# Kernel tuning notes

Hardware: AMD Instinct MI355X
Metric: run time of the kernel (lower is better)

The kernel has to match this reference:

```python
import jax, jax.numpy as jnp
import numpy as np

N = 50000          # num_nodes
E = 800000         # general (base) edge count
R_BASE = 3         # base relation types
R = 2 * R_BASE + 1 # base + inverse + self-loop relation
D_IN = 64
D_HID = 64
D_OUT = 64


def _glorot(k, shape):
    # xavier_uniform with relu gain, fan over last two dims
    gain = np.sqrt(2.0)
    bound = gain * np.sqrt(6.0 / (shape[-2] + shape[-1]))
    return jax.random.uniform(k, shape, jnp.float32, -bound, bound)


def setup_inputs() -> dict:
    key = jax.random.key(0)
    ks = jax.random.split(key, 6)
    x = jax.random.normal(ks[0], (N, D_IN), dtype=jnp.float32)
    src = jax.random.randint(ks[1], (E,), 0, N)
    dst = jax.random.randint(ks[2], (E,), 0, N)
    et = jax.random.randint(ks[3], (E,), 0, R_BASE)
    nodes = jnp.arange(N)
    # triples = [original edges, inverse edges (type+R_BASE), self-loops (type 2*R_BASE)]
    triples = jnp.concatenate([
        jnp.stack([src, et, dst], axis=1),
        jnp.stack([dst, et + R_BASE, src], axis=1),
        jnp.stack([nodes, jnp.full((N,), 2 * R_BASE), nodes], axis=1),
    ], axis=0).astype(jnp.int64)
    w1 = _glorot(ks[4], (R, D_IN, D_HID))
    w2 = _glorot(ks[5], (R, D_HID, D_OUT))
    b1 = jnp.zeros((D_HID,), jnp.float32)
    b2 = jnp.zeros((D_OUT,), jnp.float32)
    return {"x": x, "w1": w1, "b1": b1, "w2": w2, "b2": b2,
            "triples": triples, "num_nodes": N, "num_edge_types": R}


def _rgcn_layer(x, W, b, triples, num_nodes, num_rels):
    # vertical stacking: sparse adj [R*N, N], entry (r*N+src, dst) = 1, row-normalised
    src, et, dst = triples[:, 0], triples[:, 1], triples[:, 2]
    rows = et * num_nodes + src                     # [T] row index in stacked adj
    counts = jnp.zeros((num_rels * num_nodes,), x.dtype).at[rows].add(1.0)
    vals = 1.0 / counts[rows]                       # per-edge row-normalised weight
    msgs = vals[:, None] * x[dst]                   # [T, d] gathered + scaled messages
    af = jax.ops.segment_sum(msgs, rows, num_segments=num_rels * num_nodes)
    af = af.reshape(num_rels, num_nodes, x.shape[1])  # [R, N, d]
    return jnp.einsum('rio,rni->no', W, af) + b


def reference(x, w1, b1, w2, b2, triples, num_nodes, num_edge_types):
    h = _rgcn_layer(x, w1, b1, triples, num_nodes, num_edge_types)
    h = jax.nn.relu(h)
    out = _rgcn_layer(h, w2, b2, triples, num_nodes, num_edge_types)
    return out
```

## Files before the change

kernel.cpp:

```cpp
#include <hip/hip_runtime.h>
#include <stdint.h>

#define D 64
#define TILE 2048
#define PK 8
#define NBMAX 128
#define BW 512
#define RMAX 8

typedef __attribute__((ext_vector_type(8))) short bf16x8;
typedef __attribute__((ext_vector_type(4))) float f32x4;

__device__ __forceinline__ unsigned short f2bf(float f) {
    union { float f; unsigned int i; } v; v.f = f;
    unsigned int x = v.i;
    unsigned int r = (x + 0x7FFFu + ((x >> 16) & 1u)) >> 16;
    return (unsigned short)r;
}
__device__ __forceinline__ float lo_bf(unsigned int u) {
    union { unsigned int i; float f; } v; v.i = u << 16; return v.f;
}
__device__ __forceinline__ float hi_bf(unsigned int u) {
    union { unsigned int i; float f; } v; v.i = u & 0xFFFF0000u; return v.f;
}

__global__ void detect_kernel(const int* __restrict__ t32, int probe, int expect,
                              unsigned int* __restrict__ flag) {
    if (blockIdx.x == 0 && threadIdx.x == 0)
        flag[0] = (t32[probe] == expect) ? 0u : 1u;
}

__global__ void __launch_bounds__(256) binpass_kernel(const unsigned int* __restrict__ t32,
                                                      const unsigned int* __restrict__ flag,
                                                      unsigned int* __restrict__ staging,
                                                      unsigned int* __restrict__ binCnt,
                                                      int M, int NB, int CAP) {
    __shared__ unsigned int sorted[TILE];
    __shared__ unsigned char sortedb[TILE];
    __shared__ unsigned int hist[NBMAX];
    __shared__ unsigned int scan_[NBMAX];
    __shared__ unsigned int cur[NBMAX];
    __shared__ unsigned int gbase[NBMAX];

    int tid = threadIdx.x;
    int tileBase = blockIdx.x * TILE;

    for (int i = tid; i < NBMAX; i += 256) hist[i] = 0;
    __syncthreads();

    bool is64 = flag[0] != 0;
    unsigned int myE[PK];
    unsigned char myB[PK];
    #pragma unroll
    for (int k = 0; k < PK; k++) {
        int e = tileBase + tid * PK + k;
        myB[k] = 0xFF;
        if (e < M) {
            long w = (long)e * 3;
            unsigned int src, et, dst;
            if (is64) { src = t32[2*w]; et = t32[2*(w+1)]; dst = t32[2*(w+2)]; }
            else      { src = t32[w];   et = t32[w+1];     dst = t32[w+2]; }
            unsigned int b = src >> 9;
            unsigned int lsrc = src & (BW - 1);
            myE[k] = (lsrc << 20) | (et << 17) | dst;
            myB[k] = (unsigned char)b;
            atomicAdd(&hist[b], 1u);
        }
    }
    __syncthreads();

    if (tid < NBMAX) scan_[tid] = hist[tid];
    __syncthreads();
    for (int off = 1; off < NBMAX; off <<= 1) {
        unsigned int v = (tid < NBMAX && tid >= off) ? scan_[tid - off] : 0u;
        __syncthreads();
        if (tid < NBMAX) scan_[tid] += v;
        __syncthreads();
    }
    if (tid < NB) {
        gbase[tid] = atomicAdd(&binCnt[tid], hist[tid]);
        cur[tid] = scan_[tid] - hist[tid];
    }
    __syncthreads();

    #pragma unroll
    for (int k = 0; k < PK; k++) {
        if (myB[k] != 0xFF) {
            unsigned int p = atomicAdd(&cur[myB[k]], 1u);
            sorted[p] = myE[k];
            sortedb[p] = myB[k];
        }
    }
    __syncthreads();

    unsigned int total = scan_[NB - 1];
    for (unsigned int i = tid; i < total; i += 256) {
        unsigned int b = sortedb[i];
        unsigned int local = i - (scan_[b] - hist[b]);
        unsigned int slot = gbase[b] + local;
        if (slot < (unsigned int)CAP)
            staging[(size_t)b * CAP + slot] = sorted[i];
    }
}

__global__ void __launch_bounds__(512) buildcsr_kernel(const unsigned int* __restrict__ staging,
                                                       const unsigned int* __restrict__ binCnt,
                                                       unsigned int* __restrict__ segOff,
                                                       uint2* __restrict__ adj,
                                                       int M, int N, int R, int NB, int CAP) {
    __shared__ unsigned int hist7[RMAX * BW];
    __shared__ unsigned int curs7[RMAX * BW];
    __shared__ unsigned int scanbuf[BW];
    __shared__ unsigned int sbase[NBMAX];

    int b = blockIdx.x, tid = threadIdx.x;
    int nodeBase = b * BW;
    int nNodes = N - nodeBase; if (nNodes > BW) nNodes = BW;
    unsigned int cntB = binCnt[b]; if (cntB > (unsigned int)CAP) cntB = CAP;

    for (int i = tid; i < RMAX * BW; i += 512) hist7[i] = 0;
    __syncthreads();

    const unsigned int* st = staging + (size_t)b * CAP;
    for (unsigned int i = tid; i < cntB; i += 512) {
        unsigned int e = st[i];
        unsigned int lsrc = e >> 20, et = (e >> 17) & 7u;
        atomicAdd(&hist7[et * BW + lsrc], 1u);
    }
    __syncthreads();

    unsigned int d = 0;
    for (int r2 = 0; r2 < R; r2++) d += hist7[r2 * BW + tid];
    scanbuf[tid] = d;
    __syncthreads();
    for (int off = 1; off < BW; off <<= 1) {
        unsigned int v = (tid >= off) ? scanbuf[tid - off] : 0u;
        __syncthreads();
        scanbuf[tid] += v;
        __syncthreads();
    }

    if (tid < NBMAX) sbase[tid] = (tid < NB) ? min(binCnt[tid], (unsigned int)CAP) : 0u;
    __syncthreads();
    for (int off = 1; off < NBMAX; off <<= 1) {
        unsigned int v = (tid < NBMAX && tid >= off) ? sbase[tid - off] : 0u;
        __syncthreads();
        if (tid < NBMAX) sbase[tid] += v;
        __syncthreads();
    }
    unsigned int baseB = (b == 0) ? 0u : sbase[b - 1];

    unsigned int nodeStart = baseB + scanbuf[tid] - d;
    if (tid < nNodes) {
        unsigned int o = nodeStart;
        for (int et = 0; et < R; et++) {
            segOff[(size_t)(nodeBase + tid) * 8 + et] = o;
            curs7[et * BW + tid] = o;
            o += hist7[et * BW + tid];
        }
        segOff[(size_t)(nodeBase + tid) * 8 + R] = o;
    } else {
        for (int et = 0; et < R; et++) curs7[et * BW + tid] = 0;
    }
    __syncthreads();

    for (unsigned int i = tid; i < cntB; i += 512) {
        unsigned int e = st[i];
        unsigned int lsrc = e >> 20, et = (e >> 17) & 7u, dst = e & 0x1FFFFu;
        unsigned int pos = atomicAdd(&curs7[et * BW + lsrc], 1u);
        float val = 1.0f / (float)hist7[et * BW + lsrc];
        uint2 m; m.x = dst; m.y = __float_as_uint(val);
        adj[pos] = m;
    }
}

__global__ void convert_kernel(const float* __restrict__ x, unsigned short* __restrict__ xb, int total) {
    int i = (blockIdx.x * blockDim.x + threadIdx.x) * 4;
    if (i + 3 < total) {
        float4 v = *(const float4*)(x + i);
        ushort4 o; o.x = f2bf(v.x); o.y = f2bf(v.y); o.z = f2bf(v.z); o.w = f2bf(v.w);
        *(ushort4*)(xb + i) = o;
    } else {
        for (int j = i; j < total; j++) xb[j] = f2bf(x[j]);
    }
}

__global__ void packw_kernel(const float* __restrict__ W, unsigned short* __restrict__ wpack, int R) {
    int gid = blockIdx.x * blockDim.x + threadIdx.x;
    if (gid >= R * 512) return;
    int lane = gid & 63;
    int c = (gid >> 6) & 3;
    int t = (gid >> 8) & 1;
    int r = gid >> 9;
    int col = c * 16 + (lane & 15);
    int kbase = t * 32 + 8 * (lane >> 4);
    #pragma unroll
    for (int j = 0; j < 8; j++) {
        wpack[(size_t)gid * 8 + j] = f2bf(W[((size_t)r * D + kbase + j) * D + col]);
    }
}

template<int RM>
__global__ void __launch_bounds__(256) agg_kernel(const unsigned short* __restrict__ xtab,
                                                  const uint2* __restrict__ adj,
                                                  const unsigned int* __restrict__ segOff,
                                                  unsigned int* __restrict__ afcat,
                                                  int N, int totalWaves) {
    int w = blockIdx.x * 4 + (threadIdx.x >> 6);
    int lane = threadIdx.x & 63;
    int g = lane >> 4;
    int cq = lane & 15;
    const int stride = RM * 32;
    const int PERG = (2 * RM + 3) >> 2;
    int npairs = (N + 1) >> 1;

    for (int p = w; p < npairs; p += totalWaves) {
        int n0 = 2 * p;
        #pragma unroll
        for (int k = 0; k < PERG; k++) {
            int sidx = g * PERG + k;
            int node = n0 + (sidx >= RM ? 1 : 0);
            int r = sidx - (sidx >= RM ? RM : 0);
            bool valid = node < N;
            unsigned int s = 0, e = 0;
            if (valid) {
                s = segOff[(size_t)node * 8 + r];
                e = segOff[(size_t)node * 8 + r + 1];
            }
            float a0 = 0.f, a1 = 0.f, a2 = 0.f, a3 = 0.f;
            #pragma unroll 2
            for (unsigned int idx = s; idx < e; ++idx) {
                uint2 m = adj[idx];
                float val = __uint_as_float(m.y);
                uint2 u = *(const uint2*)(xtab + (size_t)m.x * D + 4 * cq);
                a0 += val * lo_bf(u.x);
                a1 += val * hi_bf(u.x);
                a2 += val * lo_bf(u.y);
                a3 += val * hi_bf(u.y);
            }
            if (valid) {
                uint2 o;
                o.x = ((unsigned int)f2bf(a1) << 16) | (unsigned int)f2bf(a0);
                o.y = ((unsigned int)f2bf(a3) << 16) | (unsigned int)f2bf(a2);
                *(uint2*)(afcat + (size_t)node * stride + r * 32 + 2 * cq) = o;
            }
        }
    }
}

__global__ void __launch_bounds__(256) agg_kernel_dyn(const unsigned short* __restrict__ xtab,
                                                      const uint2* __restrict__ adj,
                                                      const unsigned int* __restrict__ segOff,
                                                      unsigned int* __restrict__ afcat,
                                                      int N, int totalWaves, int Rm1) {
    int w = blockIdx.x * 4 + (threadIdx.x >> 6);
    int lane = threadIdx.x & 63;
    int g = lane >> 4;
    int cq = lane & 15;
    int stride = Rm1 * 32;
    int PERG = (2 * Rm1 + 3) >> 2;
    int npairs = (N + 1) >> 1;

    for (int p = w; p < npairs; p += totalWaves) {
        int n0 = 2 * p;
        for (int k = 0; k < PERG; k++) {
            int sidx = g * PERG + k;
            int node = n0 + (sidx >= Rm1 ? 1 : 0);
            int r = sidx - (sidx >= Rm1 ? Rm1 : 0);
            bool valid = (node < N) && (sidx < 2 * Rm1);
            unsigned int s = 0, e = 0;
            if (valid) {
                s = segOff[(size_t)node * 8 + r];
                e = segOff[(size_t)node * 8 + r + 1];
            }
            float a0 = 0.f, a1 = 0.f, a2 = 0.f, a3 = 0.f;
            for (unsigned int idx = s; idx < e; ++idx) {
                uint2 m = adj[idx];
                float val = __uint_as_float(m.y);
                uint2 u = *(const uint2*)(xtab + (size_t)m.x * D + 4 * cq);
                a0 += val * lo_bf(u.x);
                a1 += val * hi_bf(u.x);
                a2 += val * lo_bf(u.y);
                a3 += val * hi_bf(u.y);
            }
            if (valid) {
                uint2 o;
                o.x = ((unsigned int)f2bf(a1) << 16) | (unsigned int)f2bf(a0);
                o.y = ((unsigned int)f2bf(a3) << 16) | (unsigned int)f2bf(a2);
                *(uint2*)(afcat + (size_t)node * stride + r * 32 + 2 * cq) = o;
            }
        }
    }
}

__global__ void __launch_bounds__(256) gemm2_kernel(const unsigned short* __restrict__ afcat,
                                                    const unsigned short* __restrict__ xtab,
                                                    const unsigned short* __restrict__ wpack,
                                                    const float* __restrict__ bias,
                                                    unsigned short* __restrict__ out_bf,
                                                    float* __restrict__ out_f32,
                                                    int N, int nchunks, int mode) {
    int wid = blockIdx.x * 4 + (threadIdx.x >> 6);
    int lane = threadIdx.x & 63;
    if (wid >= nchunks) return;
    int n0 = wid * 16;
    int arow = n0 + (lane & 15);
    if (arow >= N) arow = N - 1;
    int ksub = 8 * (lane >> 4);

    bf16x8 a[14];
    const unsigned short* af = afcat + (size_t)arow * 384 + ksub;
    #pragma unroll
    for (int kt = 0; kt < 12; kt++) a[kt] = *(const bf16x8*)(af + kt * 32);
    const unsigned short* xr = xtab + (size_t)arow * D + ksub;
    a[12] = *(const bf16x8*)(xr);
    a[13] = *(const bf16x8*)(xr + 32);

    const unsigned short* wp = wpack + (size_t)lane * 8;
    int colb = lane & 15;
    int rowbase = n0 + (lane >> 4) * 4;
    #pragma unroll
    for (int c = 0; c < 4; c++) {
        f32x4 acc = {0.f, 0.f, 0.f, 0.f};
        #pragma unroll
        for (int kt = 0; kt < 14; kt++) {
            bf16x8 bfr = *(const bf16x8*)(wp + (size_t)(kt * 4 + c) * 512);
            acc = __builtin_amdgcn_mfma_f32_16x16x32_bf16(a[kt], bfr, acc, 0, 0, 0);
        }
        int col = 16 * c + colb;
        float bl = bias[col];
        #pragma unroll
        for (int q = 0; q < 4; q++) {
            int row = rowbase + q;
            if (row < N) {
                float o = acc[q] + bl;
                if (mode == 0) out_bf[(size_t)row * D + col] = f2bf(fmaxf(o, 0.f));
                else           out_f32[(size_t)row * D + col] = o;
            }
        }
    }
}

extern "C" void kernel_launch(void* const* d_in, const int* in_sizes, int n_in,
                              void* d_out, int out_size, void* d_ws, size_t ws_size,
                              hipStream_t stream) {
    const float* x  = (const float*)d_in[0];
    const float* w1 = (const float*)d_in[1];
    const float* b1 = (const float*)d_in[2];
    const float* w2 = (const float*)d_in[3];
    const float* b2 = (const float*)d_in[4];
    const int* trip = (const int*)d_in[5];

    const int N = in_sizes[0] / D;
    const int R = in_sizes[1] / (D * D);
    const int M = in_sizes[5] / 3;

    const int NB = (N + BW - 1) / BW;
    const int CAP = (((2 * (M / NB)) + 1023) / 1024) * 1024;

    char* p = (char*)d_ws;
    auto alloc = [&](size_t bytes) { void* q = (void*)p; p += (bytes + 255) / 256 * 256; return q; };
    unsigned int* binCnt  = (unsigned int*)alloc((size_t)NBMAX * 4);
    unsigned int* segOff  = (unsigned int*)alloc((size_t)N * 8 * 4);
    unsigned int* flag    = (unsigned int*)alloc(256);
    unsigned int* staging = (unsigned int*)alloc((size_t)NB * CAP * 4);
    uint2*        adj     = (uint2*)alloc((size_t)M * 8);
    unsigned int* afcat   = (unsigned int*)alloc((size_t)N * (R - 1) * 32 * 4);
    unsigned short* xb    = (unsigned short*)alloc((size_t)N * D * 2);
    unsigned short* hb    = (unsigned short*)alloc((size_t)N * D * 2);
    unsigned short* wp1   = (unsigned short*)alloc((size_t)R * 512 * 8 * 2);
    unsigned short* wp2   = (unsigned short*)alloc((size_t)R * 512 * 8 * 2);

    hipMemsetAsync(binCnt, 0, (size_t)NBMAX * 4, stream);

    int probe = (M - N) * 3 + 1;
    detect_kernel<<<1, 1, 0, stream>>>(trip, probe, R - 1, flag);

    int tiles = (M + TILE - 1) / TILE;
    binpass_kernel<<<tiles, 256, 0, stream>>>((const unsigned int*)trip, flag, staging, binCnt, M, NB, CAP);
    buildcsr_kernel<<<NB, 512, 0, stream>>>(staging, binCnt, segOff, adj, M, N, R, NB, CAP);

    int totX = N * D;
    convert_kernel<<<(totX / 4 + 255) / 256, 256, 0, stream>>>(x, xb, totX);
    packw_kernel<<<(R * 512 + 255) / 256, 256, 0, stream>>>(w1, wp1, R);
    packw_kernel<<<(R * 512 + 255) / 256, 256, 0, stream>>>(w2, wp2, R);

    int gblocks = 2048, tw = gblocks * 4;
    int nchunks = (N + 15) / 16;
    int gemmb = (nchunks + 3) / 4;

    if (R - 1 == 6)
        agg_kernel<6><<<gblocks, 256, 0, stream>>>(xb, adj, segOff, afcat, N, tw);
    else
        agg_kernel_dyn<<<gblocks, 256, 0, stream>>>(xb, adj, segOff, afcat, N, tw, R - 1);
    gemm2_kernel<<<gemmb, 256, 0, stream>>>((const unsigned short*)afcat, xb, wp1, b1, hb, nullptr, N, nchunks, 0);

    if (R - 1 == 6)
        agg_kernel<6><<<gblocks, 256, 0, stream>>>(hb, adj, segOff, afcat, N, tw);
    else
        agg_kernel_dyn<<<gblocks, 256, 0, stream>>>(hb, adj, segOff, afcat, N, tw, R - 1);
    gemm2_kernel<<<gemmb, 256, 0, stream>>>((const unsigned short*)afcat, hb, wp2, b2, nullptr, (float*)d_out, N, nchunks, 1);
}
```

Baseline: 286.5 us.

## Split feature tables into column halves and drop per-edge weights from adjacency

```diff
diff --git a/kernel.cpp b/kernel.cpp
--- a/kernel.cpp
+++ b/kernel.cpp
@@ -106,7 +106,7 @@
 __global__ void __launch_bounds__(512) buildcsr_kernel(const unsigned int* __restrict__ staging,
                                                        const unsigned int* __restrict__ binCnt,
                                                        unsigned int* __restrict__ segOff,
-                                                       uint2* __restrict__ adj,
+                                                       unsigned int* __restrict__ adj,
                                                        int M, int N, int R, int NB, int CAP) {
     __shared__ unsigned int hist7[RMAX * BW];
     __shared__ unsigned int curs7[RMAX * BW];
@@ -168,21 +168,20 @@
         unsigned int e = st[i];
         unsigned int lsrc = e >> 20, et = (e >> 17) & 7u, dst = e & 0x1FFFFu;
         unsigned int pos = atomicAdd(&curs7[et * BW + lsrc], 1u);
-        float val = 1.0f / (float)hist7[et * BW + lsrc];
-        uint2 m; m.x = dst; m.y = __float_as_uint(val);
-        adj[pos] = m;
-    }
-}
-
-__global__ void convert_kernel(const float* __restrict__ x, unsigned short* __restrict__ xb, int total) {
-    int i = (blockIdx.x * blockDim.x + threadIdx.x) * 4;
-    if (i + 3 < total) {
-        float4 v = *(const float4*)(x + i);
-        ushort4 o; o.x = f2bf(v.x); o.y = f2bf(v.y); o.z = f2bf(v.z); o.w = f2bf(v.w);
-        *(ushort4*)(xb + i) = o;
-    } else {
-        for (int j = i; j < total; j++) xb[j] = f2bf(x[j]);
-    }
+        adj[pos] = dst;
+    }
+}
+
+__global__ void convert_split_kernel(const float* __restrict__ x,
+                                     unsigned short* __restrict__ xbL,
+                                     unsigned short* __restrict__ xbH, int N) {
+    int gid = blockIdx.x * blockDim.x + threadIdx.x;
+    if (gid >= N * 16) return;
+    int n = gid >> 4, half = (gid >> 3) & 1, q = gid & 7;
+    float4 v = *(const float4*)(x + (size_t)n * 64 + half * 32 + q * 4);
+    ushort4 o; o.x = f2bf(v.x); o.y = f2bf(v.y); o.z = f2bf(v.z); o.w = f2bf(v.w);
+    unsigned short* dst = half ? xbH : xbL;
+    *(ushort4*)(dst + (size_t)n * 32 + q * 4) = o;
 }
 
 __global__ void packw_kernel(const float* __restrict__ W, unsigned short* __restrict__ wpack, int R) {
@@ -201,17 +200,17 @@
 }
 
 template<int RM>
-__global__ void __launch_bounds__(256) agg_kernel(const unsigned short* __restrict__ xtab,
-                                                  const uint2* __restrict__ adj,
+__global__ void __launch_bounds__(256) agg_kernel(const unsigned short* __restrict__ xh,
+                                                  const unsigned int* __restrict__ adj,
                                                   const unsigned int* __restrict__ segOff,
-                                                  unsigned int* __restrict__ afcat,
+                                                  unsigned int* __restrict__ afh,
                                                   int N, int totalWaves) {
     int w = blockIdx.x * 4 + (threadIdx.x >> 6);
     int lane = threadIdx.x & 63;
     int g = lane >> 4;
     int cq = lane & 15;
+    const int PERG = (2 * RM + 3) >> 2;
     const int stride = RM * 32;
-    const int PERG = (2 * RM + 3) >> 2;
     int npairs = (N + 1) >> 1;
 
     for (int p = w; p < npairs; p += totalWaves) {
@@ -227,38 +226,34 @@
                 s = segOff[(size_t)node * 8 + r];
                 e = segOff[(size_t)node * 8 + r + 1];
             }
-            float a0 = 0.f, a1 = 0.f, a2 = 0.f, a3 = 0.f;
-            #pragma unroll 2
+            float a0 = 0.f, a1 = 0.f;
+            #pragma unroll 4
             for (unsigned int idx = s; idx < e; ++idx) {
-                uint2 m = adj[idx];
-                float val = __uint_as_float(m.y);
-                uint2 u = *(const uint2*)(xtab + (size_t)m.x * D + 4 * cq);
-                a0 += val * lo_bf(u.x);
-                a1 += val * hi_bf(u.x);
-                a2 += val * lo_bf(u.y);
-                a3 += val * hi_bf(u.y);
+                unsigned int dst = __builtin_nontemporal_load(&adj[idx]);
+                unsigned int u = *(const unsigned int*)(xh + (size_t)dst * 32 + 2 * cq);
+                a0 += lo_bf(u);
+                a1 += hi_bf(u);
             }
             if (valid) {
-                uint2 o;
-                o.x = ((unsigned int)f2bf(a1) << 16) | (unsigned int)f2bf(a0);
-                o.y = ((unsigned int)f2bf(a3) << 16) | (unsigned int)f2bf(a2);
-                *(uint2*)(afcat + (size_t)node * stride + r * 32 + 2 * cq) = o;
-            }
-        }
-    }
-}
-
-__global__ void __launch_bounds__(256) agg_kernel_dyn(const unsigned short* __restrict__ xtab,
-                                                      const uint2* __restrict__ adj,
+                float val = (e > s) ? 1.0f / (float)(e - s) : 0.f;
+                unsigned int o = ((unsigned int)f2bf(a1 * val) << 16) | (unsigned int)f2bf(a0 * val);
+                __builtin_nontemporal_store(o, &afh[(size_t)node * stride + 32 * r + cq]);
+            }
+        }
+    }
+}
+
+__global__ void __launch_bounds__(256) agg_kernel_dyn(const unsigned short* __restrict__ xh,
+                                                      const unsigned int* __restrict__ adj,
                                                       const unsigned int* __restrict__ segOff,
-                                                      unsigned int* __restrict__ afcat,
+                                                      unsigned int* __restrict__ afh,
                                                       int N, int totalWaves, int Rm1) {
     int w = blockIdx.x * 4 + (threadIdx.x >> 6);
     int lane = threadIdx.x & 63;
     int g = lane >> 4;
     int cq = lane & 15;
+    int PERG = (2 * Rm1 + 3) >> 2;
     int stride = Rm1 * 32;
-    int PERG = (2 * Rm1 + 3) >> 2;
     int npairs = (N + 1) >> 1;
 
     for (int p = w; p < npairs; p += totalWaves) {
@@ -273,31 +268,29 @@
                 s = segOff[(size_t)node * 8 + r];
                 e = segOff[(size_t)node * 8 + r + 1];
             }
-            float a0 = 0.f, a1 = 0.f, a2 = 0.f, a3 = 0.f;
+            float a0 = 0.f, a1 = 0.f;
             for (unsigned int idx = s; idx < e; ++idx) {
-                uint2 m = adj[idx];
-                float val = __uint_as_float(m.y);
-                uint2 u = *(const uint2*)(xtab + (size_t)m.x * D + 4 * cq);
-                a0 += val * lo_bf(u.x);
-                a1 += val * hi_bf(u.x);
-                a2 += val * lo_bf(u.y);
-                a3 += val * hi_bf(u.y);
+                unsigned int dst = adj[idx];
+                unsigned int u = *(const unsigned int*)(xh + (size_t)dst * 32 + 2 * cq);
+                a0 += lo_bf(u);
+                a1 += hi_bf(u);
             }
             if (valid) {
-                uint2 o;
-                o.x = ((unsigned int)f2bf(a1) << 16) | (unsigned int)f2bf(a0);
-                o.y = ((unsigned int)f2bf(a3) << 16) | (unsigned int)f2bf(a2);
-                *(uint2*)(afcat + (size_t)node * stride + r * 32 + 2 * cq) = o;
+                float val = (e > s) ? 1.0f / (float)(e - s) : 0.f;
+                unsigned int o = ((unsigned int)f2bf(a1 * val) << 16) | (unsigned int)f2bf(a0 * val);
+                afh[(size_t)node * stride + 32 * r + cq] = o;
             }
         }
     }
 }
 
 __global__ void __launch_bounds__(256) gemm2_kernel(const unsigned short* __restrict__ afcat,
-                                                    const unsigned short* __restrict__ xtab,
+                                                    const unsigned short* __restrict__ xbL,
+                                                    const unsigned short* __restrict__ xbH,
                                                     const unsigned short* __restrict__ wpack,
                                                     const float* __restrict__ bias,
-                                                    unsigned short* __restrict__ out_bf,
+                                                    unsigned short* __restrict__ outL,
+                                                    unsigned short* __restrict__ outH,
                                                     float* __restrict__ out_f32,
                                                     int N, int nchunks, int mode) {
     int wid = blockIdx.x * 4 + (threadIdx.x >> 6);
@@ -312,9 +305,8 @@
     const unsigned short* af = afcat + (size_t)arow * 384 + ksub;
     #pragma unroll
     for (int kt = 0; kt < 12; kt++) a[kt] = *(const bf16x8*)(af + kt * 32);
-    const unsigned short* xr = xtab + (size_t)arow * D + ksub;
-    a[12] = *(const bf16x8*)(xr);
-    a[13] = *(const bf16x8*)(xr + 32);
+    a[12] = *(const bf16x8*)(xbL + (size_t)arow * 32 + ksub);
+    a[13] = *(const bf16x8*)(xbH + (size_t)arow * 32 + ksub);
 
     const unsigned short* wp = wpack + (size_t)lane * 8;
     int colb = lane & 15;
@@ -334,8 +326,12 @@
             int row = rowbase + q;
             if (row < N) {
                 float o = acc[q] + bl;
-                if (mode == 0) out_bf[(size_t)row * D + col] = f2bf(fmaxf(o, 0.f));
-                else           out_f32[(size_t)row * D + col] = o;
+                if (mode == 0) {
+                    unsigned short* dst = (c < 2) ? outL : outH;
+                    dst[(size_t)row * 32 + (col & 31)] = f2bf(fmaxf(o, 0.f));
+                } else {
+                    out_f32[(size_t)row * D + col] = o;
+                }
             }
         }
     }
@@ -364,10 +360,12 @@
     unsigned int* segOff  = (unsigned int*)alloc((size_t)N * 8 * 4);
     unsigned int* flag    = (unsigned int*)alloc(256);
     unsigned int* staging = (unsigned int*)alloc((size_t)NB * CAP * 4);
-    uint2*        adj     = (uint2*)alloc((size_t)M * 8);
+    unsigned int* adj     = (unsigned int*)alloc((size_t)M * 4);
     unsigned int* afcat   = (unsigned int*)alloc((size_t)N * (R - 1) * 32 * 4);
-    unsigned short* xb    = (unsigned short*)alloc((size_t)N * D * 2);
-    unsigned short* hb    = (unsigned short*)alloc((size_t)N * D * 2);
+    unsigned short* xbL   = (unsigned short*)alloc((size_t)N * 32 * 2);
+    unsigned short* xbH   = (unsigned short*)alloc((size_t)N * 32 * 2);
+    unsigned short* hbL   = (unsigned short*)alloc((size_t)N * 32 * 2);
+    unsigned short* hbH   = (unsigned short*)alloc((size_t)N * 32 * 2);
     unsigned short* wp1   = (unsigned short*)alloc((size_t)R * 512 * 8 * 2);
     unsigned short* wp2   = (unsigned short*)alloc((size_t)R * 512 * 8 * 2);
 
@@ -380,8 +378,7 @@
     binpass_kernel<<<tiles, 256, 0, stream>>>((const unsigned int*)trip, flag, staging, binCnt, M, NB, CAP);
     buildcsr_kernel<<<NB, 512, 0, stream>>>(staging, binCnt, segOff, adj, M, N, R, NB, CAP);
 
-    int totX = N * D;
-    convert_kernel<<<(totX / 4 + 255) / 256, 256, 0, stream>>>(x, xb, totX);
+    convert_split_kernel<<<(N * 16 + 255) / 256, 256, 0, stream>>>(x, xbL, xbH, N);
     packw_kernel<<<(R * 512 + 255) / 256, 256, 0, stream>>>(w1, wp1, R);
     packw_kernel<<<(R * 512 + 255) / 256, 256, 0, stream>>>(w2, wp2, R);
 
@@ -389,15 +386,23 @@
     int nchunks = (N + 15) / 16;
     int gemmb = (nchunks + 3) / 4;
 
-    if (R - 1 == 6)
-        agg_kernel<6><<<gblocks, 256, 0, stream>>>(xb, adj, segOff, afcat, N, tw);
-    else
-        agg_kernel_dyn<<<gblocks, 256, 0, stream>>>(xb, adj, segOff, afcat, N, tw, R - 1);
-    gemm2_kernel<<<gemmb, 256, 0, stream>>>((const unsigned short*)afcat, xb, wp1, b1, hb, nullptr, N, nchunks, 0);
-
-    if (R - 1 == 6)
-        agg_kernel<6><<<gblocks, 256, 0, stream>>>(hb, adj, segOff, afcat, N, tw);
-    else
-        agg_kernel_dyn<<<gblocks, 256, 0, stream>>>(hb, adj, segOff, afcat, N, tw, R - 1);
-    gemm2_kernel<<<gemmb, 256, 0, stream>>>((const unsigned short*)afcat, hb, wp2, b2, nullptr, (float*)d_out, N, nchunks, 1);
-}
+    if (R - 1 == 6) {
+        agg_kernel<6><<<gblocks, 256, 0, stream>>>(xbL, adj, segOff, afcat,      N, tw);
+        agg_kernel<6><<<gblocks, 256, 0, stream>>>(xbH, adj, segOff, afcat + 16, N, tw);
+    } else {
+        agg_kernel_dyn<<<gblocks, 256, 0, stream>>>(xbL, adj, segOff, afcat,      N, tw, R - 1);
+        agg_kernel_dyn<<<gblocks, 256, 0, stream>>>(xbH, adj, segOff, afcat + 16, N, tw, R - 1);
+    }
+    gemm2_kernel<<<gemmb, 256, 0, stream>>>((const unsigned short*)afcat, xbL, xbH, wp1, b1,
+                                            hbL, hbH, nullptr, N, nchunks, 0);
+
+    if (R - 1 == 6) {
+        agg_kernel<6><<<gblocks, 256, 0, stream>>>(hbL, adj, segOff, afcat,      N, tw);
+        agg_kernel<6><<<gblocks, 256, 0, stream>>>(hbH, adj, segOff, afcat + 16, N, tw);
+    } else {
+        agg_kernel_dyn<<<gblocks, 256, 0, stream>>>(hbL, adj, segOff, afcat,      N, tw, R - 1);
+        agg_kernel_dyn<<<gblocks, 256, 0, stream>>>(hbH, adj, segOff, afcat + 16, N, tw, R - 1);
+    }
+    gemm2_kernel<<<gemmb, 256, 0, stream>>>((const unsigned short*)afcat, hbL, hbH, wp2, b2,
+                                            nullptr, nullptr, (float*)d_out, N, nchunks, 1);
+}
```

Measured after the change: 372.6 us. 1.3x slower.
